# Performance work log

Measured on AMD Instinct MI355X. Metric: run time of the kernel, lower is better.

## Reference

```python
import jax, jax.numpy as jnp
import numpy as np

H = 8      # num_attention_heads
DH = 96    # attention_head_size
LN_EPS = 1e-5


def setup_inputs() -> dict:
    key = jax.random.key(0)
    ks = jax.random.split(key, 12)
    B, S, D = 2, 768, 768
    sc = 0.02
    return {
        "hidden_states": jax.random.normal(ks[0], (B, S, D), jnp.float32),
        "distance_matrix": jax.random.uniform(ks[1], (B, S, S), jnp.float32) * 20.0,
        "angle_matrix": jax.random.uniform(ks[2], (B, S, S), jnp.float32) * np.pi,
        "attention_mask": jnp.ones((B, S), jnp.float32),
        "Wq": jax.random.normal(ks[3], (D, D), jnp.float32) * sc,
        "bq": jnp.zeros((D,), jnp.float32),
        "Wk": jax.random.normal(ks[4], (D, D), jnp.float32) * sc,
        "bk": jnp.zeros((D,), jnp.float32),
        "Wv": jax.random.normal(ks[5], (D, D), jnp.float32) * sc,
        "bv": jnp.zeros((D,), jnp.float32),
        "Wd": jax.random.normal(ks[6], (DH,), jnp.float32) * sc,
        "bd": jnp.zeros((DH,), jnp.float32),
        "Wa": jax.random.normal(ks[7], (DH,), jnp.float32) * sc,
        "ba": jnp.zeros((DH,), jnp.float32),
        "Wo": jax.random.normal(ks[8], (D, D), jnp.float32) * sc,
        "bo": jnp.zeros((D,), jnp.float32),
        "ln_g": jnp.ones((D,), jnp.float32),
        "ln_b": jnp.zeros((D,), jnp.float32),
    }


def _heads(x, B, S):
    # [B,S,D] -> [B,H,S,DH]
    return x.reshape(B, S, H, DH).transpose(0, 2, 1, 3)


def reference(hidden_states, distance_matrix, angle_matrix, attention_mask,
              Wq, bq, Wk, bk, Wv, bv, Wd, bd, Wa, ba, Wo, bo, ln_g, ln_b):
    B, S, D = hidden_states.shape
    q = _heads(hidden_states @ Wq.T + bq, B, S)   # [B,H,S,DH]
    k = _heads(hidden_states @ Wk.T + bk, B, S)
    v = _heads(hidden_states @ Wv.T + bv, B, S)

    scores = jnp.einsum('bhid,bhjd->bhij', q, k) / jnp.sqrt(jnp.float32(DH))

    # distance / angle relative-position biases: emb[b,i,j,:] = dist[b,i,j]*Wd + bd
    dist_emb = distance_matrix[..., None] * Wd + bd   # [B,S,S,DH]
    scores = scores + jnp.einsum('bhid,bijd->bhij', q, dist_emb)
    ang_emb = angle_matrix[..., None] * Wa + ba       # [B,S,S,DH]
    scores = scores + jnp.einsum('bhid,bijd->bhij', q, ang_emb)

    # key mask, broadcast over heads and query positions
    scores = scores + (1.0 - attention_mask)[:, None, None, :] * -10000.0

    probs = jax.nn.softmax(scores, axis=-1)           # [B,H,S,S]
    ctx = jnp.einsum('bhij,bhjd->bhid', probs, v)
    ctx = ctx.transpose(0, 2, 1, 3).reshape(B, S, D)  # [B,S,D]

    out = ctx @ Wo.T + bo
    x = out + hidden_states
    mu = jnp.mean(x, axis=-1, keepdims=True)
    var = jnp.var(x, axis=-1, keepdims=True)
    out = (x - mu) * jax.lax.rsqrt(var + LN_EPS) * ln_g + ln_b
    return out, probs
```

## Files before the change

kernel.cpp:

```cpp
#include <hip/hip_runtime.h>
#include <stdint.h>

#define B_  2
#define S_  768
#define D_  768
#define H_  8
#define DH_ 96

typedef unsigned short ushort_t;
typedef __bf16 bf16x8 __attribute__((ext_vector_type(8)));
typedef float  f32x4  __attribute__((ext_vector_type(4)));
typedef _Float16 f16x4 __attribute__((ext_vector_type(4)));

__device__ inline ushort_t f2bf(float f) {
    union { float f; unsigned int u; } v; v.f = f;
    unsigned int u = v.u;
    unsigned int r = u + 0x7fffu + ((u >> 16) & 1u);
    return (ushort_t)(r >> 16);
}
__device__ inline float bf2f(ushort_t u) {
    union { unsigned int i; float f; } c; c.i = ((unsigned int)u) << 16;
    return c.f;
}
__device__ inline ushort_t f2h(float f) {
    union { _Float16 h; ushort_t u; } c; c.h = (_Float16)f; return c.u;
}

__device__ inline void glds16(const void* gp, void* lp) {
    auto g = reinterpret_cast<const __attribute__((address_space(1))) uint32_t*>(
        reinterpret_cast<uintptr_t>(gp));
    auto l = reinterpret_cast<__attribute__((address_space(3))) uint32_t*>(
        reinterpret_cast<uintptr_t>(lp));
    __builtin_amdgcn_global_load_lds(g, l, 16, 0, 0);
}

#define SBAR()  { __builtin_amdgcn_sched_barrier(0); __builtin_amdgcn_s_barrier(); \
                  __builtin_amdgcn_sched_barrier(0); }
#define WAIT_VM(N) { asm volatile("s_waitcnt vmcnt(" #N ")" ::: "memory"); \
                     __builtin_amdgcn_sched_barrier(0); }
#define WAIT_LGKM0() { asm volatile("s_waitcnt lgkmcnt(0)" ::: "memory"); \
                       __builtin_amdgcn_sched_barrier(0); }

__global__ __launch_bounds__(256) void k_convert(
        const float* __restrict__ X, const float* __restrict__ Wq,
        const float* __restrict__ Wk, const float* __restrict__ Wv,
        const float* __restrict__ Wo, const float* __restrict__ distm,
        const float* __restrict__ angm,
        ushort_t* __restrict__ Xb, ushort_t* __restrict__ Wb,
        ushort_t* __restrict__ Dh, ushort_t* __restrict__ Ah) {
    const int NX4 = (B_ * S_ * D_) / 4;
    const int NW4 = (D_ * D_) / 4;
    const int NWall = 4 * NW4;
    const int ND4 = (B_ * S_ * S_) / 4;
    int i = blockIdx.x * blockDim.x + threadIdx.x;
    float4 v;
    ushort_t* dst;
    bool h16 = false;
    if (i < NX4) {
        v = ((const float4*)X)[i];
        dst = Xb + i * 4;
    } else if (i < NX4 + NWall) {
        int wi = i - NX4;
        int sel = wi / NW4;
        int off = wi - sel * NW4;
        const float* src = (sel == 0) ? Wq : (sel == 1) ? Wk : (sel == 2) ? Wv : Wo;
        v = ((const float4*)src)[off];
        dst = Wb + wi * 4;
    } else if (i < NX4 + NWall + ND4) {
        int off = i - NX4 - NWall;
        v = ((const float4*)distm)[off];
        dst = Dh + off * 4; h16 = true;
    } else {
        int off = i - NX4 - NWall - ND4;
        v = ((const float4*)angm)[off];
        dst = Ah + off * 4; h16 = true;
    }
    ushort4 o;
    if (h16) { o.x = f2h(v.x); o.y = f2h(v.y); o.z = f2h(v.z); o.w = f2h(v.w); }
    else     { o.x = f2bf(v.x); o.y = f2bf(v.y); o.z = f2bf(v.z); o.w = f2bf(v.w); }
    *(ushort4*)dst = o;
}

__device__ inline void gemm64_dbuf(
        const ushort_t* __restrict__ A, int lda,
        const ushort_t* __restrict__ Bt, int ldb,
        int K, int m0, int n0,
        ushort_t* As, ushort_t* Bs, f32x4 acc[2][2]) {
    const int tid  = threadIdx.x;
    const int lane = tid & 63, wave = tid >> 6;
    const int wm = (wave >> 1) * 32, wn = (wave & 1) * 32;
    const int fr = lane & 15, fk = (lane >> 4) * 8;
    const ushort_t* Ap = A  + (size_t)(m0 + wave * 16 + (lane >> 2)) * lda + (lane & 3) * 8;
    const ushort_t* Bp = Bt + (size_t)(n0 + wave * 16 + (lane >> 2)) * ldb + (lane & 3) * 8;
    glds16(Ap, As + wave * 512);
    glds16(Bp, Bs + wave * 512);
    for (int kt = 0; kt < K; kt += 32) {
        const int cur = (kt >> 5) & 1;
        if (kt + 32 < K) {
            glds16(Ap + kt + 32, As + (cur ^ 1) * 2048 + wave * 512);
            glds16(Bp + kt + 32, Bs + (cur ^ 1) * 2048 + wave * 512);
            WAIT_VM(2)
        } else {
            WAIT_VM(0)
        }
        SBAR()
        const ushort_t* Ab = As + cur * 2048;
        const ushort_t* Bb = Bs + cur * 2048;
        bf16x8 a0 = *(const bf16x8*)&Ab[(wm      + fr) * 32 + fk];
        bf16x8 a1 = *(const bf16x8*)&Ab[(wm + 16 + fr) * 32 + fk];
        bf16x8 b0 = *(const bf16x8*)&Bb[(wn      + fr) * 32 + fk];
        bf16x8 b1 = *(const bf16x8*)&Bb[(wn + 16 + fr) * 32 + fk];
        acc[0][0] = __builtin_amdgcn_mfma_f32_16x16x32_bf16(a0, b0, acc[0][0], 0, 0, 0);
        acc[0][1] = __builtin_amdgcn_mfma_f32_16x16x32_bf16(a0, b1, acc[0][1], 0, 0, 0);
        acc[1][0] = __builtin_amdgcn_mfma_f32_16x16x32_bf16(a1, b0, acc[1][0], 0, 0, 0);
        acc[1][1] = __builtin_amdgcn_mfma_f32_16x16x32_bf16(a1, b1, acc[1][1], 0, 0, 0);
        WAIT_LGKM0()
        SBAR()
    }
}

__global__ __launch_bounds__(256) void k_qkv(
        const ushort_t* __restrict__ Xb, const ushort_t* __restrict__ Wb,
        const float* __restrict__ bq, const float* __restrict__ bk,
        const float* __restrict__ bv,
        ushort_t* __restrict__ Qb, ushort_t* __restrict__ Kb,
        ushort_t* __restrict__ Vtb) {
    __shared__ __align__(16) ushort_t As[2 * 64 * 32];
    __shared__ __align__(16) ushort_t Bs[2 * 64 * 32];
    f32x4 acc[2][2];
    #pragma unroll
    for (int i = 0; i < 2; i++)
        #pragma unroll
        for (int j = 0; j < 2; j++) acc[i][j] = (f32x4){0.f, 0.f, 0.f, 0.f};
    const int m0 = blockIdx.y * 64, n0 = blockIdx.x * 64;
    gemm64_dbuf(Xb, D_, Wb, D_, D_, m0, n0, As, Bs, acc);
    const int lane = threadIdx.x & 63, wave = threadIdx.x >> 6;
    const int wm = (wave >> 1) * 32, wn = (wave & 1) * 32;
    #pragma unroll
    for (int ni = 0; ni < 2; ni++) {
        int gcol = n0 + wn + ni * 16 + (lane & 15);
        int gsel = gcol / D_, d768 = gcol - gsel * D_;
        int h = d768 / DH_, d = d768 - h * DH_;
        float bias = (gsel == 0 ? bq : (gsel == 1 ? bk : bv))[d768];
        #pragma unroll
        for (int mi = 0; mi < 2; mi++) {
            int grow0 = m0 + wm + mi * 16 + (lane >> 4) * 4;
            int b = grow0 / S_, s0 = grow0 - b * S_;
            int bh = b * H_ + h;
            if (gsel == 2) {
                ushort4 o4;
                o4.x = f2bf(acc[mi][ni][0] + bias);
                o4.y = f2bf(acc[mi][ni][1] + bias);
                o4.z = f2bf(acc[mi][ni][2] + bias);
                o4.w = f2bf(acc[mi][ni][3] + bias);
                *(ushort4*)&Vtb[((size_t)bh * DH_ + d) * S_ + s0] = o4;
            } else if (gsel == 1) {
                #pragma unroll
                for (int r = 0; r < 4; r++)
                    Kb[(((size_t)bh * 12 + (d >> 3)) * S_ + s0 + r) * 8 + (d & 7)] =
                        f2bf(acc[mi][ni][r] + bias);
            } else {
                #pragma unroll
                for (int r = 0; r < 4; r++)
                    Qb[((size_t)bh * S_ + s0 + r) * DH_ + d] = f2bf(acc[mi][ni][r] + bias);
            }
        }
    }
}

__global__ __launch_bounds__(256, 3) void k_flash(
        const ushort_t* __restrict__ Qb, const ushort_t* __restrict__ Kb,
        const ushort_t* __restrict__ Vtb,
        const float* __restrict__ Wd, const float* __restrict__ bd,
        const float* __restrict__ Wa, const float* __restrict__ ba,
        const ushort_t* __restrict__ Dh, const ushort_t* __restrict__ Ah,
        const float* __restrict__ mask,
        float* __restrict__ probs, ushort_t* __restrict__ Ctxb) {
    __shared__ float mstat[64];
    __shared__ float lstat[64];
    __shared__ float ctxred[1600];
    const int idx = blockIdx.x;
    const int bh = idx & 15, t = idx >> 4;
    const int b = bh >> 3, h = bh & 7;
    const int r0 = t * 16;
    const int tid = threadIdx.x, lane = tid & 63, w = tid >> 6;
    const int frn = lane & 15, g = lane >> 4;
    const ushort_t* Qbh = Qb + (size_t)bh * S_ * DH_;
    const ushort_t* Kbh = Kb + (size_t)bh * 12 * S_ * 8;
    const ushort_t* Vbh = Vtb + (size_t)bh * DH_ * S_;

    #pragma unroll
    for (int i = 0; i < 7; ++i) {
        int z = tid + i * 256;
        if (z < 1600) ctxred[z] = 0.f;
    }

    bf16x8 aq0, aq1, aq2;
    {
        const ushort_t* qp = Qbh + (size_t)(r0 + frn) * DH_ + g * 8;
        aq0 = *(const bf16x8*)qp;
        aq1 = *(const bf16x8*)(qp + 32);
        aq2 = *(const bf16x8*)(qp + 64);
    }
    float qc0 = 0.f, qc1 = 0.f, qc2 = 0.f;
    #pragma unroll
    for (int f = 0; f < 3; ++f) {
        bf16x8 aq = (f == 0) ? aq0 : (f == 1) ? aq1 : aq2;
        #pragma unroll
        for (int e = 0; e < 8; ++e) {
            int d = f * 32 + g * 8 + e;
            float qv = (float)aq[e];
            qc0 += qv * Wd[d];
            qc1 += qv * Wa[d];
            qc2 += qv * (bd[d] + ba[d]);
        }
    }
    qc0 += __shfl_xor(qc0, 16); qc0 += __shfl_xor(qc0, 32);
    qc1 += __shfl_xor(qc1, 16); qc1 += __shfl_xor(qc1, 32);
    qc2 += __shfl_xor(qc2, 16); qc2 += __shfl_xor(qc2, 32);

    const float isq = 0.10206207261596577f;

    f32x4 acc[12];
    const ushort_t* kbase = Kbh + ((size_t)g * S_ + 16 * w + frn) * 8;
    const ushort_t* dbase = Dh + (size_t)(b * S_ + r0 + frn) * S_ + w * 16 + g * 4;
    const ushort_t* abase = Ah + (size_t)(b * S_ + r0 + frn) * S_ + w * 16 + g * 4;
    const float*    mbase = mask + b * S_ + w * 16 + g * 4;
    #pragma unroll
    for (int c = 0; c < 12; ++c) {
        const ushort_t* kp = kbase + (size_t)c * 64 * 8;
        bf16x8 k0 = *(const bf16x8*)kp;
        bf16x8 k1 = *(const bf16x8*)(kp + (size_t)4 * S_ * 8);
        bf16x8 k2 = *(const bf16x8*)(kp + (size_t)8 * S_ * 8);
        union { uint2 u; f16x4 hh; } dd, aa;
        dd.u = *(const uint2*)(dbase + c * 64);
        aa.u = *(const uint2*)(abase + c * 64);
        float4 m4 = *(const float4*)(mbase + c * 64);
        f32x4 ca = (f32x4){0.f, 0.f, 0.f, 0.f};
        ca = __builtin_amdgcn_mfma_f32_16x16x32_bf16(k0, aq0, ca, 0, 0, 0);
        ca = __builtin_amdgcn_mfma_f32_16x16x32_bf16(k1, aq1, ca, 0, 0, 0);
        ca = __builtin_amdgcn_mfma_f32_16x16x32_bf16(k2, aq2, ca, 0, 0, 0);
        f32x4 o;
        o[0] = ca[0] * isq + (float)dd.hh[0] * qc0 + (float)aa.hh[0] * qc1 + qc2 + (1.f - m4.x) * -10000.f;
        o[1] = ca[1] * isq + (float)dd.hh[1] * qc0 + (float)aa.hh[1] * qc1 + qc2 + (1.f - m4.y) * -10000.f;
        o[2] = ca[2] * isq + (float)dd.hh[2] * qc0 + (float)aa.hh[2] * qc1 + qc2 + (1.f - m4.z) * -10000.f;
        o[3] = ca[3] * isq + (float)dd.hh[3] * qc0 + (float)aa.hh[3] * qc1 + qc2 + (1.f - m4.w) * -10000.f;
        acc[c] = o;
    }

    float mx = -1e30f;
    #pragma unroll
    for (int c = 0; c < 12; ++c)
        #pragma unroll
        for (int r = 0; r < 4; ++r) mx = fmaxf(mx, acc[c][r]);
    mx = fmaxf(mx, __shfl_xor(mx, 16));
    mx = fmaxf(mx, __shfl_xor(mx, 32));
    if (g == 0) mstat[w * 16 + frn] = mx;
    __syncthreads();
    float mf = fmaxf(fmaxf(mstat[frn], mstat[16 + frn]),
                     fmaxf(mstat[32 + frn], mstat[48 + frn]));
    float sum = 0.f;
    #pragma unroll
    for (int c = 0; c < 12; ++c)
        #pragma unroll
        for (int r = 0; r < 4; ++r) {
            float e = __expf(acc[c][r] - mf);
            acc[c][r] = e;
            sum += e;
        }
    sum += __shfl_xor(sum, 16);
    sum += __shfl_xor(sum, 32);
    if (g == 0) lstat[w * 16 + frn] = sum;
    __syncthreads();
    float inv = 1.f / (lstat[frn] + lstat[16 + frn] + lstat[32 + frn] + lstat[48 + frn]);

    f32x4 accO[6];
    #pragma unroll
    for (int i = 0; i < 6; ++i) accO[i] = (f32x4){0.f, 0.f, 0.f, 0.f};
    float* prow = probs + ((size_t)bh * S_ + r0 + frn) * S_ + w * 16 + g * 4;
    const ushort_t* vbase0 = Vbh + (size_t)frn * S_ + w * 16 + g * 4;
    #pragma unroll
    for (int p = 0; p < 6; ++p) {
        const int c = 2 * p;
        const ushort_t* vb_p = vbase0 + p * 128;
        uint2 v0[6], v1[6];
        #pragma unroll
        for (int nt = 0; nt < 6; ++nt) {
            v0[nt] = *(const uint2*)(vb_p + (size_t)nt * 16 * S_);
            v1[nt] = *(const uint2*)(vb_p + (size_t)nt * 16 * S_ + 64);
        }
        float4 pw;
        pw.x = acc[c][0] * inv; pw.y = acc[c][1] * inv;
        pw.z = acc[c][2] * inv; pw.w = acc[c][3] * inv;
        *(float4*)(prow + c * 64) = pw;
        pw.x = acc[c + 1][0] * inv; pw.y = acc[c + 1][1] * inv;
        pw.z = acc[c + 1][2] * inv; pw.w = acc[c + 1][3] * inv;
        *(float4*)(prow + (c + 1) * 64) = pw;
        union { bf16x8 v; ushort_t u[8]; } pa;
        #pragma unroll
        for (int r = 0; r < 4; ++r) {
            pa.u[r]     = f2bf(acc[c][r]);
            pa.u[r + 4] = f2bf(acc[c + 1][r]);
        }
        #pragma unroll
        for (int nt = 0; nt < 6; ++nt) {
            union { bf16x8 v; uint2 q2[2]; } vb;
            vb.q2[0] = v0[nt];
            vb.q2[1] = v1[nt];
            accO[nt] = __builtin_amdgcn_mfma_f32_16x16x32_bf16(pa.v, vb.v, accO[nt], 0, 0, 0);
        }
    }

    #pragma unroll
    for (int nt = 0; nt < 6; ++nt)
        #pragma unroll
        for (int r = 0; r < 4; ++r)
            atomicAdd(&ctxred[(4 * g + r) * 100 + nt * 16 + frn], accO[nt][r]);
    __syncthreads();
    {
        int zr = tid >> 4, zc = tid & 15;
        float ivr = 1.f / (lstat[zr] + lstat[16 + zr] + lstat[32 + zr] + lstat[48 + zr]);
        ushort_t* crow = Ctxb + ((size_t)b * S_ + r0 + zr) * D_ + h * DH_;
        #pragma unroll
        for (int i = 0; i < 6; ++i)
            crow[i * 16 + zc] = f2bf(ctxred[zr * 100 + i * 16 + zc] * ivr);
    }
}

__global__ __launch_bounds__(256) void k_out(
        const ushort_t* __restrict__ Ctxb, const ushort_t* __restrict__ Wob,
        const float* __restrict__ bo, const float* __restrict__ hidden,
        float* __restrict__ xbuf) {
    __shared__ __align__(16) ushort_t As[2 * 64 * 32];
    __shared__ __align__(16) ushort_t Bs[2 * 64 * 32];
    f32x4 acc[2][2];
    #pragma unroll
    for (int i = 0; i < 2; i++)
        #pragma unroll
        for (int j = 0; j < 2; j++) acc[i][j] = (f32x4){0.f, 0.f, 0.f, 0.f};
    const int m0 = blockIdx.y * 64, n0 = blockIdx.x * 64;
    gemm64_dbuf(Ctxb, D_, Wob, D_, D_, m0, n0, As, Bs, acc);
    const int lane = threadIdx.x & 63, wave = threadIdx.x >> 6;
    const int wm = (wave >> 1) * 32, wn = (wave & 1) * 32;
    #pragma unroll
    for (int ni = 0; ni < 2; ni++) {
        int gcol = n0 + wn + ni * 16 + (lane & 15);
        float bias = bo[gcol];
        #pragma unroll
        for (int mi = 0; mi < 2; mi++) {
            #pragma unroll
            for (int r = 0; r < 4; r++) {
                int grow = m0 + wm + mi * 16 + (lane >> 4) * 4 + r;
                xbuf[(size_t)grow * D_ + gcol] =
                    acc[mi][ni][r] + bias + hidden[(size_t)grow * D_ + gcol];
            }
        }
    }
}

__global__ __launch_bounds__(256) void k_ln(
        const float* __restrict__ xbuf, const float* __restrict__ g,
        const float* __restrict__ bb, float* __restrict__ out) {
    const float* x = xbuf + (size_t)blockIdx.x * D_;
    const int t = threadIdx.x;
    float a0 = x[t], a1 = x[t + 256], a2 = x[t + 512];
    float s = a0 + a1 + a2;
    float ss = a0 * a0 + a1 * a1 + a2 * a2;
    __shared__ float r1[4], r2[4];
    #pragma unroll
    for (int o = 32; o > 0; o >>= 1) { s += __shfl_down(s, o); ss += __shfl_down(ss, o); }
    if ((t & 63) == 0) { r1[t >> 6] = s; r2[t >> 6] = ss; }
    __syncthreads();
    float ts = r1[0] + r1[1] + r1[2] + r1[3];
    float tss = r2[0] + r2[1] + r2[2] + r2[3];
    float mu = ts * (1.0f / D_);
    float var = tss * (1.0f / D_) - mu * mu;
    float rstd = rsqrtf(var + 1e-5f);
    float* o = out + (size_t)blockIdx.x * D_;
    o[t]       = (a0 - mu) * rstd * g[t]       + bb[t];
    o[t + 256] = (a1 - mu) * rstd * g[t + 256] + bb[t + 256];
    o[t + 512] = (a2 - mu) * rstd * g[t + 512] + bb[t + 512];
}

extern "C" void kernel_launch(void* const* d_in, const int* in_sizes, int n_in,
                              void* d_out, int out_size, void* d_ws, size_t ws_size,
                              hipStream_t stream) {
    const float* X     = (const float*)d_in[0];
    const float* distm = (const float*)d_in[1];
    const float* angm  = (const float*)d_in[2];
    const float* mask  = (const float*)d_in[3];
    const float* Wq    = (const float*)d_in[4];
    const float* bq    = (const float*)d_in[5];
    const float* Wk    = (const float*)d_in[6];
    const float* bk    = (const float*)d_in[7];
    const float* Wv    = (const float*)d_in[8];
    const float* bv    = (const float*)d_in[9];
    const float* Wd    = (const float*)d_in[10];
    const float* bd    = (const float*)d_in[11];
    const float* Wa    = (const float*)d_in[12];
    const float* ba    = (const float*)d_in[13];
    const float* Wo    = (const float*)d_in[14];
    const float* bo    = (const float*)d_in[15];
    const float* ln_g  = (const float*)d_in[16];
    const float* ln_b  = (const float*)d_in[17];

    float* outp  = (float*)d_out;
    float* probs = (float*)d_out + (size_t)B_ * S_ * D_;

    char* ws = (char*)d_ws;
    ushort_t* Xb    = (ushort_t*)(ws + 0);
    ushort_t* Wb    = (ushort_t*)(ws + 2359296);
    ushort_t* Qb    = (ushort_t*)(ws + 7077888);
    ushort_t* Kb    = (ushort_t*)(ws + 9437184);
    ushort_t* Vtb   = (ushort_t*)(ws + 11796480);
    ushort_t* Ctxb  = (ushort_t*)(ws + 14155776);
    float*    xbuf  = (float*)   (ws + 16662528);
    ushort_t* Dh    = (ushort_t*)(ws + 16662528);
    ushort_t* Ah    = (ushort_t*)(ws + 16662528 + 2359296);

    k_convert<<<5760, 256, 0, stream>>>(X, Wq, Wk, Wv, Wo, distm, angm, Xb, Wb, Dh, Ah);
    k_qkv<<<dim3(36, 24), 256, 0, stream>>>(Xb, Wb, bq, bk, bv, Qb, Kb, Vtb);
    k_flash<<<768, 256, 0, stream>>>(Qb, Kb, Vtb, Wd, bd, Wa, ba, Dh, Ah, mask, probs, Ctxb);
    k_out<<<dim3(12, 24), 256, 0, stream>>>(Ctxb, Wb + (size_t)2304 * 768, bo, X, xbuf);
    k_ln<<<1536, 256, 0, stream>>>(xbuf, ln_g, ln_b, outp);
}
```

Measured before the change: 202.8 us.

## Retile distance/angle and V buffers so flash kernel loads are contiguous

The convert kernel now transposes the distance and angle matrices through LDS into a tiled fp16 layout grouped by 4-column chunks. The flash kernel can then read the bias values with coalesced accesses along the query-row axis. The QKV epilogue writes V in a fragment-ordered layout, so each lane fetches one 16-byte bf16x8 MFMA operand instead of two 8-byte loads. The cost is an LDS transpose in the convert stage and scattered V stores in the GEMM epilogue.

```diff
diff --git a/kernel.cpp b/kernel.cpp
--- a/kernel.cpp
+++ b/kernel.cpp
@@ -48,37 +48,62 @@
         const float* __restrict__ angm,
         ushort_t* __restrict__ Xb, ushort_t* __restrict__ Wb,
         ushort_t* __restrict__ Dh, ushort_t* __restrict__ Ah) {
+    __shared__ float tlds[64][65];
     const int NX4 = (B_ * S_ * D_) / 4;
     const int NW4 = (D_ * D_) / 4;
-    const int NWall = 4 * NW4;
-    const int ND4 = (B_ * S_ * S_) / 4;
-    int i = blockIdx.x * blockDim.x + threadIdx.x;
-    float4 v;
-    ushort_t* dst;
-    bool h16 = false;
-    if (i < NX4) {
-        v = ((const float4*)X)[i];
-        dst = Xb + i * 4;
-    } else if (i < NX4 + NWall) {
-        int wi = i - NX4;
-        int sel = wi / NW4;
-        int off = wi - sel * NW4;
-        const float* src = (sel == 0) ? Wq : (sel == 1) ? Wk : (sel == 2) ? Wv : Wo;
-        v = ((const float4*)src)[off];
-        dst = Wb + wi * 4;
-    } else if (i < NX4 + NWall + ND4) {
-        int off = i - NX4 - NWall;
-        v = ((const float4*)distm)[off];
-        dst = Dh + off * 4; h16 = true;
-    } else {
-        int off = i - NX4 - NWall - ND4;
-        v = ((const float4*)angm)[off];
-        dst = Ah + off * 4; h16 = true;
-    }
-    ushort4 o;
-    if (h16) { o.x = f2h(v.x); o.y = f2h(v.y); o.z = f2h(v.z); o.w = f2h(v.w); }
-    else     { o.x = f2bf(v.x); o.y = f2bf(v.y); o.z = f2bf(v.z); o.w = f2bf(v.w); }
-    *(ushort4*)dst = o;
+    const int bid = blockIdx.x, tid = threadIdx.x;
+    if (bid < 3456) {
+        int i = bid * 256 + tid;
+        float4 v;
+        ushort_t* dst;
+        if (i < NX4) {
+            v = ((const float4*)X)[i];
+            dst = Xb + i * 4;
+        } else {
+            int wi = i - NX4;
+            int sel = wi / NW4;
+            int off = wi - sel * NW4;
+            const float* src = (sel == 0) ? Wq : (sel == 1) ? Wk : (sel == 2) ? Wv : Wo;
+            v = ((const float4*)src)[off];
+            dst = Wb + wi * 4;
+        }
+        ushort4 o;
+        o.x = f2bf(v.x); o.y = f2bf(v.y); o.z = f2bf(v.z); o.w = f2bf(v.w);
+        *(ushort4*)dst = o;
+        return;
+    }
+    int tidx = bid - 3456;
+    int mat = tidx / 288, t2 = tidx - mat * 288;
+    int b = t2 / 144, t3 = t2 - b * 144;
+    int rt = t3 / 12, ct = t3 - rt * 12;
+    const float* src = (mat ? angm : distm) + ((size_t)(b * S_ + rt * 64)) * S_ + ct * 64;
+    ushort_t* dstm = mat ? Ah : Dh;
+    {
+        int tr = tid >> 4, tc4 = tid & 15;
+        #pragma unroll
+        for (int k = 0; k < 4; ++k) {
+            int row = tr + k * 16;
+            float4 v4 = *(const float4*)(src + (size_t)row * S_ + tc4 * 4);
+            tlds[row][tc4 * 4 + 0] = v4.x;
+            tlds[row][tc4 * 4 + 1] = v4.y;
+            tlds[row][tc4 * 4 + 2] = v4.z;
+            tlds[row][tc4 * 4 + 3] = v4.w;
+        }
+    }
+    __syncthreads();
+    {
+        int row = tid & 63, s4b = tid >> 6;
+        #pragma unroll
+        for (int k = 0; k < 4; ++k) {
+            int s4l = s4b * 4 + k;
+            ushort4 o4;
+            o4.x = f2h(tlds[row][s4l * 4 + 0]);
+            o4.y = f2h(tlds[row][s4l * 4 + 1]);
+            o4.z = f2h(tlds[row][s4l * 4 + 2]);
+            o4.w = f2h(tlds[row][s4l * 4 + 3]);
+            *(ushort4*)&dstm[(((size_t)b * 192 + ct * 16 + s4l) * 768 + rt * 64 + row) * 4] = o4;
+        }
+    }
 }
 
 __device__ inline void gemm64_dbuf(
@@ -153,7 +178,11 @@
                 o4.y = f2bf(acc[mi][ni][1] + bias);
                 o4.z = f2bf(acc[mi][ni][2] + bias);
                 o4.w = f2bf(acc[mi][ni][3] + bias);
-                *(ushort4*)&Vtb[((size_t)bh * DH_ + d) * S_ + s0] = o4;
+                int p = s0 >> 7, wv = (s0 >> 4) & 3, gq = (s0 >> 2) & 3;
+                int e0 = (s0 >> 6) & 1;
+                size_t off = ((size_t)bh * 73728) + p * 12288 + wv * 3072
+                           + (d >> 4) * 512 + (gq * 16 + (d & 15)) * 8 + e0 * 4;
+                *(ushort4*)&Vtb[off] = o4;
             } else if (gsel == 1) {
                 #pragma unroll
                 for (int r = 0; r < 4; r++)
@@ -187,7 +216,6 @@
     const int frn = lane & 15, g = lane >> 4;
     const ushort_t* Qbh = Qb + (size_t)bh * S_ * DH_;
     const ushort_t* Kbh = Kb + (size_t)bh * 12 * S_ * 8;
-    const ushort_t* Vbh = Vtb + (size_t)bh * DH_ * S_;
 
     #pragma unroll
     for (int i = 0; i < 7; ++i) {
@@ -223,8 +251,8 @@
 
     f32x4 acc[12];
     const ushort_t* kbase = Kbh + ((size_t)g * S_ + 16 * w + frn) * 8;
-    const ushort_t* dbase = Dh + (size_t)(b * S_ + r0 + frn) * S_ + w * 16 + g * 4;
-    const ushort_t* abase = Ah + (size_t)(b * S_ + r0 + frn) * S_ + w * 16 + g * 4;
+    const ushort_t* dbase = Dh + ((size_t)(b * 192 + w * 4 + g) * 768 + r0 + frn) * 4;
+    const ushort_t* abase = Ah + ((size_t)(b * 192 + w * 4 + g) * 768 + r0 + frn) * 4;
     const float*    mbase = mask + b * S_ + w * 16 + g * 4;
     #pragma unroll
     for (int c = 0; c < 12; ++c) {
@@ -233,8 +261,8 @@
         bf16x8 k1 = *(const bf16x8*)(kp + (size_t)4 * S_ * 8);
         bf16x8 k2 = *(const bf16x8*)(kp + (size_t)8 * S_ * 8);
         union { uint2 u; f16x4 hh; } dd, aa;
-        dd.u = *(const uint2*)(dbase + c * 64);
-        aa.u = *(const uint2*)(abase + c * 64);
+        dd.u = *(const uint2*)(dbase + (size_t)c * 16 * 768 * 4);
+        aa.u = *(const uint2*)(abase + (size_t)c * 16 * 768 * 4);
         float4 m4 = *(const float4*)(mbase + c * 64);
         f32x4 ca = (f32x4){0.f, 0.f, 0.f, 0.f};
         ca = __builtin_amdgcn_mfma_f32_16x16x32_bf16(k0, aq0, ca, 0, 0, 0);
@@ -278,17 +306,14 @@
     #pragma unroll
     for (int i = 0; i < 6; ++i) accO[i] = (f32x4){0.f, 0.f, 0.f, 0.f};
     float* prow = probs + ((size_t)bh * S_ + r0 + frn) * S_ + w * 16 + g * 4;
-    const ushort_t* vbase0 = Vbh + (size_t)frn * S_ + w * 16 + g * 4;
+    const ushort_t* vfb = Vtb + (size_t)bh * 73728 + w * 3072 + lane * 8;
     #pragma unroll
     for (int p = 0; p < 6; ++p) {
         const int c = 2 * p;
-        const ushort_t* vb_p = vbase0 + p * 128;
-        uint2 v0[6], v1[6];
-        #pragma unroll
-        for (int nt = 0; nt < 6; ++nt) {
-            v0[nt] = *(const uint2*)(vb_p + (size_t)nt * 16 * S_);
-            v1[nt] = *(const uint2*)(vb_p + (size_t)nt * 16 * S_ + 64);
-        }
+        bf16x8 vfrag[6];
+        #pragma unroll
+        for (int nt = 0; nt < 6; ++nt)
+            vfrag[nt] = *(const bf16x8*)(vfb + p * 12288 + nt * 512);
         float4 pw;
         pw.x = acc[c][0] * inv; pw.y = acc[c][1] * inv;
         pw.z = acc[c][2] * inv; pw.w = acc[c][3] * inv;
@@ -303,12 +328,8 @@
             pa.u[r + 4] = f2bf(acc[c + 1][r]);
         }
         #pragma unroll
-        for (int nt = 0; nt < 6; ++nt) {
-            union { bf16x8 v; uint2 q2[2]; } vb;
-            vb.q2[0] = v0[nt];
-            vb.q2[1] = v1[nt];
-            accO[nt] = __builtin_amdgcn_mfma_f32_16x16x32_bf16(pa.v, vb.v, accO[nt], 0, 0, 0);
-        }
+        for (int nt = 0; nt < 6; ++nt)
+            accO[nt] = __builtin_amdgcn_mfma_f32_16x16x32_bf16(pa.v, vfrag[nt], accO[nt], 0, 0, 0);
     }
 
     #pragma unroll
@@ -418,7 +439,7 @@
     ushort_t* Dh    = (ushort_t*)(ws + 16662528);
     ushort_t* Ah    = (ushort_t*)(ws + 16662528 + 2359296);
 
-    k_convert<<<5760, 256, 0, stream>>>(X, Wq, Wk, Wv, Wo, distm, angm, Xb, Wb, Dh, Ah);
+    k_convert<<<4032, 256, 0, stream>>>(X, Wq, Wk, Wv, Wo, distm, angm, Xb, Wb, Dh, Ah);
     k_qkv<<<dim3(36, 24), 256, 0, stream>>>(Xb, Wb, bq, bk, bv, Qb, Kb, Vtb);
     k_flash<<<768, 256, 0, stream>>>(Qb, Kb, Vtb, Wd, bd, Wa, ba, Dh, Ah, mask, probs, Ctxb);
     k_out<<<dim3(12, 24), 256, 0, stream>>>(Ctxb, Wb + (size_t)2304 * 768, bo, X, xbuf);
```

Result: faster. 182.5 us (-10.0%).
